# Kernel optimization log

Hardware: AMD Instinct MI355X
Metric: run time of the kernel (lower is better)

## Reference

```python
import jax, jax.numpy as jnp
import numpy as np

B, C, D_EMB = 512, 100000, 128
SCALE = 3.0
EPS = 1e-5


def _l2norm(x, eps=1e-12):
    # matches torch F.normalize(p=2, dim=-1)
    n = jnp.sqrt(jnp.sum(x * x, axis=-1, keepdims=True))
    return x / jnp.maximum(n, eps)


def setup_inputs() -> dict:
    key = jax.random.key(0)
    k1, k2, k3 = jax.random.split(key, 3)
    X = jax.random.normal(k1, (B, D_EMB), dtype=jnp.float32)
    indices = jnp.arange(B, dtype=jnp.int64)
    T = jax.random.randint(k2, (B,), 0, C).astype(jnp.int64)
    proxies = jax.random.normal(k3, (C, D_EMB), dtype=jnp.float32) / 8.0
    return {"X": X, "indices": indices, "T": T, "proxies": proxies}


def reference(X, indices, T, proxies):
    P = _l2norm(proxies)            # (C, D)
    Xn = _l2norm(X)                 # (B, D)

    # cross_attention -----------------------------------------------------
    Pb = P[T]                       # (B, D) gather of class proxies
    # affinity2boundary[b,k] = relu(<(Pb[b]+Pb[k])/2, Xn[k]>)
    #   = relu(0.5 * ((Pb @ Xn.T)[b,k] + diag[k]))  -- avoids (B,B,D) intermediate
    diag = jnp.sum(Pb * Xn, axis=-1)                       # (B,)
    aff2b = jax.nn.relu(0.5 * (Pb @ Xn.T + diag[None, :]))  # (B, B)
    aff2x = jax.nn.relu(Xn @ Xn.T)                          # (B, B)
    attention = aff2b + aff2x

    # NOTE: faithful to torch broadcasting: (B,B) / (B,) divides by COLUMN sums
    attention = attention / (attention.sum(-1) + EPS)       # (B, B)
    attention_weights = attention @ Xn                      # (B, D)
    X2 = Xn + attention_weights

    Ps = SCALE * _l2norm(P)         # (C, D), rows have norm SCALE
    Xs = SCALE * _l2norm(X2)        # (B, D)

    # squared pairwise distance block between X rows and proxy rows
    sx = jnp.sum(Xs * Xs, axis=-1)  # (B,)
    sp = jnp.sum(Ps * Ps, axis=-1)  # (C,)
    Dm = jnp.maximum(sx[:, None] + sp[None, :] - 2.0 * (Xs @ Ps.T), 0.0)  # (B, C)

    # one-hot targets (smoothing_const = 0) with masked log-softmax
    lsm = jax.nn.log_softmax(-Dm, axis=-1)                  # (B, C)
    loss = -lsm[jnp.arange(B), T]                           # (B,)
    return loss.mean()
```

## Files before the change

### kernel.cpp

```cpp
#include <hip/hip_runtime.h>
#include <hip/hip_bf16.h>
#include <math.h>

#define B_N 512
#define C_N 100000
#define CPAD 100032
#define D_N 128
#define NCHUNK (CPAD / 64)
#define K6_GX 256
#define K6_BLOCKS K6_GX
#define PAD_CORR (32.0f * 1.522998e-8f)

typedef short short8 __attribute__((ext_vector_type(8)));
typedef float f32x4 __attribute__((ext_vector_type(4)));

__device__ __forceinline__ unsigned short f2bf(float f) {
  unsigned int u = __float_as_uint(f);
  u += 0x7fffu + ((u >> 16) & 1u);
  return (unsigned short)(u >> 16);
}

__device__ __forceinline__ unsigned int pk2bf(float lo, float hi) {
  return (unsigned int)f2bf(lo) | ((unsigned int)f2bf(hi) << 16);
}

__device__ __forceinline__ void gl_lds16(const void* g, void* l) {
  __builtin_amdgcn_global_load_lds(
      (const __attribute__((address_space(1))) void*)g,
      (__attribute__((address_space(3))) void*)l, 16, 0, 0);
}

template <int NT>
__device__ __forceinline__ float block_reduce_sum(float v, float* red) {
  int t = threadIdx.x;
  __syncthreads();
  red[t] = v;
  __syncthreads();
#pragma unroll
  for (int s = NT / 2; s > 0; s >>= 1) {
    if (t < s) red[t] += red[t + s];
    __syncthreads();
  }
  return red[0];
}

__global__ __launch_bounds__(256) void kX(const float* __restrict__ X,
                                          const float* __restrict__ proxies,
                                          const int* __restrict__ T,
                                          float* __restrict__ Xn, float* __restrict__ Pb,
                                          float* __restrict__ diagv,
                                          int* __restrict__ ctrs) {
  __shared__ float red[256];
  int b = blockIdx.x;
  int t = threadIdx.x;
  bool act = t < D_N;
  float v = act ? X[b * D_N + t] : 0.f;
  float ss = block_reduce_sum<256>(v * v, red);
  float xn = v / fmaxf(sqrtf(ss), 1e-12f);
  if (act) Xn[b * D_N + t] = xn;
  int row = T[b];
  float p = act ? proxies[(size_t)row * D_N + t] : 0.f;
  float ss2 = block_reduce_sum<256>(p * p, red);
  float pn = p / fmaxf(sqrtf(ss2), 1e-12f);
  if (act) Pb[b * D_N + t] = pn;
  float d = block_reduce_sum<256>(pn * xn, red);
  if (t == 0) {
    diagv[b] = d;
    if (b == 0) ctrs[32] = 0;
  }
}

__global__ __launch_bounds__(512) void k3_att(const float* __restrict__ Xn,
                                              const float* __restrict__ Pb,
                                              const float* __restrict__ diagv,
                                              float* __restrict__ A, float* __restrict__ S) {
  __shared__ float xb[128], pbv[128];
  __shared__ float red[512];
  int b = blockIdx.x, t = threadIdx.x;
  if (t < 128) {
    xb[t] = Xn[b * D_N + t];
    pbv[t] = Pb[b * D_N + t];
  }
  __syncthreads();
  const float4* xr = (const float4*)(Xn + (size_t)t * D_N);
  float d1 = 0.f, d2 = 0.f;
#pragma unroll
  for (int i = 0; i < 32; i++) {
    float4 v = xr[i];
    d1 += pbv[4 * i] * v.x + pbv[4 * i + 1] * v.y + pbv[4 * i + 2] * v.z + pbv[4 * i + 3] * v.w;
    d2 += xb[4 * i] * v.x + xb[4 * i + 1] * v.y + xb[4 * i + 2] * v.z + xb[4 * i + 3] * v.w;
  }
  float a = fmaxf(0.5f * (d1 + diagv[t]), 0.f) + fmaxf(d2, 0.f);
  A[(size_t)b * B_N + t] = a;
  float rs = block_reduce_sum<512>(a, red);
  if (t == 0) S[b] = rs;
}

__global__ __launch_bounds__(512) void k4ab(const float* __restrict__ Xn,
                                            const float* __restrict__ Pb,
                                            const float* __restrict__ A,
                                            const float* __restrict__ S,
                                            unsigned short* __restrict__ Xsb,
                                            float* __restrict__ lossT,
                                            float* __restrict__ sumexpP) {
  __shared__ float xb[128], pbv[128];
  __shared__ float aw[512];
  __shared__ float red[512];
  int b = blockIdx.x, t = threadIdx.x;
  if (t < 128) {
    xb[t] = Xn[b * D_N + t];
    pbv[t] = Pb[b * D_N + t];
  }
  aw[t] = A[(size_t)b * B_N + t] / (S[t] + 1e-5f);
  __syncthreads();

  int d = t & 127, h = t >> 7;
  const float* xp = Xn + (size_t)(128 * h) * D_N + d;
  const float* awp = aw + 128 * h;
  float a0 = 0.f, a1 = 0.f, a2 = 0.f, a3 = 0.f;
#pragma unroll 8
  for (int kk = 0; kk < 128; kk += 4) {
    a0 = fmaf(awp[kk], xp[(size_t)kk * D_N], a0);
    a1 = fmaf(awp[kk + 1], xp[(size_t)(kk + 1) * D_N], a1);
    a2 = fmaf(awp[kk + 2], xp[(size_t)(kk + 2) * D_N], a2);
    a3 = fmaf(awp[kk + 3], xp[(size_t)(kk + 3) * D_N], a3);
  }
  red[t] = (a0 + a1) + (a2 + a3);
  __syncthreads();
  float x2 = (t < 128) ? (xb[t] + red[t] + red[t + 128] + red[t + 256] + red[t + 384]) : 0.f;

  float ss = block_reduce_sum<512>(x2 * x2, red);
  float xs = 3.f * x2 / fmaxf(sqrtf(ss), 1e-12f);
  if (t < 128) Xsb[b * D_N + t] = f2bf(xs);
  float dt = block_reduce_sum<512>((t < 128) ? xs * pbv[t] : 0.f, red);
  if (t == 0) {
    lossT[b] = fmaxf(18.f - 6.f * dt, 0.f);
    sumexpP[b * 16] = 0.f;
  }
}

__global__ __launch_bounds__(512, 2) void k6_big(const float* __restrict__ proxies,
                                                 const unsigned short* __restrict__ Xsb,
                                                 float* __restrict__ sumexpP,
                                                 const float* __restrict__ lossT,
                                                 int* __restrict__ ctrs,
                                                 float* __restrict__ out) {
  __shared__ __align__(16) float fP[2][64 * 128];
  __shared__ __align__(16) unsigned short sP[64 * 128];
  __shared__ float redf[512];
  __shared__ int sLast;
  const int t = threadIdx.x;
  const int w = t >> 6;
  const int lane = t & 63;
  const int lc = lane & 15;
  const int q = lane >> 4;

  short8 afr[4][4];
#pragma unroll
  for (int mt = 0; mt < 4; mt++)
#pragma unroll
    for (int ks = 0; ks < 4; ks++)
      afr[mt][ks] = *(const short8*)(Xsb + (size_t)(64 * w + 16 * mt + lc) * D_N +
                                     ks * 32 + q * 8);

  float pe[4][4];
#pragma unroll
  for (int mt = 0; mt < 4; mt++)
#pragma unroll
    for (int r = 0; r < 4; r++) pe[mt][r] = 0.f;

  const int srow = 8 * w + (lane >> 5);
  const int scol = (lane & 31) * 4;
#define STAGEF(c0_, buf_)                                                             \
  {                                                                                   \
    _Pragma("unroll") for (int j = 0; j < 4; j++) {                                   \
      int gr = (c0_) + srow + 2 * j;                                                  \
      gr = gr < C_N ? gr : (C_N - 1);               \
      gl_lds16(proxies + (size_t)gr * D_N + scol,                                     \
               &fP[buf_][(8 * w + 2 * j) * D_N]);                                     \
    }                                                                                 \
  }

  const int cr = t >> 3;
  const int cs = t & 7;

  int cc = blockIdx.x;
  STAGEF(cc * 64, 0);
  int buf = 0;
  while (true) {
    int nc = cc + gridDim.x;
    if (nc < NCHUNK) {
      STAGEF(nc * 64, buf ^ 1);
      __builtin_amdgcn_sched_barrier(0);
      __builtin_amdgcn_s_waitcnt(0x0F74);
    } else {
      __builtin_amdgcn_sched_barrier(0);
      __builtin_amdgcn_s_waitcnt(0x0F70);
    }
    __builtin_amdgcn_sched_barrier(0);

    {
      const float* src = &fP[buf][cr * D_N + cs * 16];
      float4 v0 = ((const float4*)src)[0];
      float4 v1 = ((const float4*)src)[1];
      float4 v2 = ((const float4*)src)[2];
      float4 v3 = ((const float4*)src)[3];
      float s0 = v0.x * v0.x + v0.y * v0.y + v0.z * v0.z + v0.w * v0.w;
      float s1 = v1.x * v1.x + v1.y * v1.y + v1.z * v1.z + v1.w * v1.w;
      float s2 = v2.x * v2.x + v2.y * v2.y + v2.z * v2.z + v2.w * v2.w;
      float s3 = v3.x * v3.x + v3.y * v3.y + v3.z * v3.z + v3.w * v3.w;
      float ss = (s0 + s1) + (s2 + s3);
      ss += __shfl_xor(ss, 1);
      ss += __shfl_xor(ss, 2);
      ss += __shfl_xor(ss, 4);
      float inv = 1.f / fmaxf(sqrtf(ss), 1e-12f);
      if (cc * 64 + cr >= C_N) inv = 0.f;
      uint4 g0, g1;
      g0.x = pk2bf(v0.x * inv, v0.y * inv);
      g0.y = pk2bf(v0.z * inv, v0.w * inv);
      g0.z = pk2bf(v1.x * inv, v1.y * inv);
      g0.w = pk2bf(v1.z * inv, v1.w * inv);
      g1.x = pk2bf(v2.x * inv, v2.y * inv);
      g1.y = pk2bf(v2.z * inv, v2.w * inv);
      g1.z = pk2bf(v3.x * inv, v3.y * inv);
      g1.w = pk2bf(v3.z * inv, v3.w * inv);
      int P0 = (2 * cs) ^ (cr & 15);
      int P1 = (2 * cs + 1) ^ (cr & 15);
      *(uint4*)&sP[cr * D_N + P0 * 8] = g0;
      *(uint4*)&sP[cr * D_N + P1 * 8] = g1;
    }
    __builtin_amdgcn_s_waitcnt(0xC07F);
    __builtin_amdgcn_s_barrier();
    __builtin_amdgcn_sched_barrier(0);

    f32x4 acc[4][4];
#pragma unroll
    for (int mt = 0; mt < 4; mt++)
#pragma unroll
      for (int nt = 0; nt < 4; nt++) acc[mt][nt] = (f32x4){0.f, 0.f, 0.f, 0.f};

#pragma unroll
    for (int ks = 0; ks < 4; ks++) {
      short8 bfr[4];
#pragma unroll
      for (int nt = 0; nt < 4; nt++) {
        int R = 16 * nt + lc;
        int g = (ks * 4 + q) ^ lc;
        bfr[nt] = *(const short8*)(&sP[R * 128 + (g << 3)]);
      }
#pragma unroll
      for (int nt = 0; nt < 4; nt++)
#pragma unroll
        for (int mt = 0; mt < 4; mt++)
          acc[mt][nt] = __builtin_amdgcn_mfma_f32_16x16x32_bf16(afr[mt][ks], bfr[nt],
                                                                acc[mt][nt], 0, 0, 0);
    }

#pragma unroll
    for (int mt = 0; mt < 4; mt++)
#pragma unroll
      for (int nt = 0; nt < 4; nt++) {
        f32x4 a = acc[mt][nt];
#pragma unroll
        for (int r = 0; r < 4; r++)
          pe[mt][r] += __builtin_amdgcn_exp2f(
              fminf(__fmaf_rn(8.65617024533378f, a[r], -25.9685107360013f), 0.f));
      }

    if (nc >= NCHUNK) break;
    __builtin_amdgcn_sched_barrier(0);
    __builtin_amdgcn_s_barrier();
    cc = nc;
    buf ^= 1;
  }

#pragma unroll
  for (int mt = 0; mt < 4; mt++) {
#pragma unroll
    for (int r = 0; r < 4; r++) {
      float p = pe[mt][r];
      p += __shfl_xor(p, 1);
      p += __shfl_xor(p, 2);
      p += __shfl_xor(p, 4);
      p += __shfl_xor(p, 8);
      if (lc == 0) {
        int rb = 64 * w + 16 * mt + 4 * q + r;
        atomicAdd(&sumexpP[rb * 16], p);
      }
    }
  }

  __builtin_amdgcn_s_waitcnt(0);
  if (t == 0) sLast = atomicAdd(&ctrs[32], 1);
  __syncthreads();
  if (sLast == K6_BLOCKS - 1) {
    float se = __hip_atomic_load(&sumexpP[t * 16], __ATOMIC_RELAXED,
                                 __HIP_MEMORY_SCOPE_AGENT);
    float v = lossT[t] + logf(se - PAD_CORR);
    float s = block_reduce_sum<512>(v, redf);
    if (t == 0) out[0] = s * (1.0f / 512.0f);
  }
}

extern "C" void kernel_launch(void* const* d_in, const int* in_sizes, int n_in,
                              void* d_out, int out_size, void* d_ws, size_t ws_size,
                              hipStream_t stream) {
  const float* X = (const float*)d_in[0];
  const int* T = (const int*)d_in[2];
  const float* proxies = (const float*)d_in[3];
  float* out = (float*)d_out;

  char* ws = (char*)d_ws;
  float* Xn = (float*)(ws + (size_t)CPAD * D_N * 2);
  float* Pb = Xn + B_N * D_N;
  float* X2 = Pb + B_N * D_N;
  float* dg = X2 + B_N * D_N;
  float* S = dg + B_N;
  float* lossT = S + B_N;
  float* sumexpP = lossT + B_N;
  unsigned short* Xsb = (unsigned short*)(sumexpP + B_N * 16);
  float* A = (float*)(Xsb + B_N * D_N);
  int* ctrs = (int*)(A + B_N * B_N);

  kX<<<B_N, 256, 0, stream>>>(X, proxies, T, Xn, Pb, dg, ctrs);
  k3_att<<<B_N, 512, 0, stream>>>(Xn, Pb, dg, A, S);
  k4ab<<<B_N, 512, 0, stream>>>(Xn, Pb, A, S, Xsb, lossT, sumexpP);
  k6_big<<<K6_GX, 512, 0, stream>>>(proxies, Xsb, sumexpP, lossT, ctrs, out);
}
```

Measured before the change: 142.3 us.

## Double-buffer bf16 proxy tile, assign contiguous chunks, shrink accumulators and kX block

The bf16 proxy tile in LDS now has two buffers, so the trailing barrier at the end of each chunk iteration can be dropped. Each block now handles a fixed, contiguous range of 6 or 7 chunks instead of a grid-strided sequence. The MFMA loop now runs with the column tile outermost, so only 4 accumulators are live at a time and the exp-sum epilogue is applied per column tile, which lowers register pressure. kX now launches 128 threads instead of 256, removing idle lanes. The extra LDS buffer costs 16 KB per block, which could limit how many blocks fit on a CU.

```diff
diff --git a/kernel.cpp b/kernel.cpp
--- a/kernel.cpp
+++ b/kernel.cpp
@@ -44,26 +44,25 @@
   return red[0];
 }
 
-__global__ __launch_bounds__(256) void kX(const float* __restrict__ X,
+__global__ __launch_bounds__(128) void kX(const float* __restrict__ X,
                                           const float* __restrict__ proxies,
                                           const int* __restrict__ T,
                                           float* __restrict__ Xn, float* __restrict__ Pb,
                                           float* __restrict__ diagv,
                                           int* __restrict__ ctrs) {
-  __shared__ float red[256];
+  __shared__ float red[128];
   int b = blockIdx.x;
   int t = threadIdx.x;
-  bool act = t < D_N;
-  float v = act ? X[b * D_N + t] : 0.f;
-  float ss = block_reduce_sum<256>(v * v, red);
+  float v = X[b * D_N + t];
+  float ss = block_reduce_sum<128>(v * v, red);
   float xn = v / fmaxf(sqrtf(ss), 1e-12f);
-  if (act) Xn[b * D_N + t] = xn;
+  Xn[b * D_N + t] = xn;
   int row = T[b];
-  float p = act ? proxies[(size_t)row * D_N + t] : 0.f;
-  float ss2 = block_reduce_sum<256>(p * p, red);
+  float p = proxies[(size_t)row * D_N + t];
+  float ss2 = block_reduce_sum<128>(p * p, red);
   float pn = p / fmaxf(sqrtf(ss2), 1e-12f);
-  if (act) Pb[b * D_N + t] = pn;
-  float d = block_reduce_sum<256>(pn * xn, red);
+  Pb[b * D_N + t] = pn;
+  float d = block_reduce_sum<128>(pn * xn, red);
   if (t == 0) {
     diagv[b] = d;
     if (b == 0) ctrs[32] = 0;
@@ -146,7 +145,7 @@
                                                  int* __restrict__ ctrs,
                                                  float* __restrict__ out) {
   __shared__ __align__(16) float fP[2][64 * 128];
-  __shared__ __align__(16) unsigned short sP[64 * 128];
+  __shared__ __align__(16) unsigned short sP[2][64 * 128];
   __shared__ float redf[512];
   __shared__ int sLast;
   const int t = threadIdx.x;
@@ -184,13 +183,16 @@
   const int cr = t >> 3;
   const int cs = t & 7;
 
-  int cc = blockIdx.x;
-  STAGEF(cc * 64, 0);
-  int buf = 0;
-  while (true) {
-    int nc = cc + gridDim.x;
-    if (nc < NCHUNK) {
-      STAGEF(nc * 64, buf ^ 1);
+  const int bid = blockIdx.x;
+  const int start = bid * 6 + (bid < 27 ? bid : 27);
+  const int nch = 6 + (bid < 27 ? 1 : 0);
+
+  STAGEF(start * 64, 0);
+  int fbuf = 0, sbuf = 0;
+  for (int k = 0; k < nch; k++) {
+    const int cc = start + k;
+    if (k + 1 < nch) {
+      STAGEF((cc + 1) * 64, fbuf ^ 1);
       __builtin_amdgcn_sched_barrier(0);
       __builtin_amdgcn_s_waitcnt(0x0F74);
     } else {
@@ -200,7 +202,7 @@
     __builtin_amdgcn_sched_barrier(0);
 
     {
-      const float* src = &fP[buf][cr * D_N + cs * 16];
+      const float* src = &fP[fbuf][cr * D_N + cs * 16];
       float4 v0 = ((const float4*)src)[0];
       float4 v1 = ((const float4*)src)[1];
       float4 v2 = ((const float4*)src)[2];
@@ -226,52 +228,40 @@
       g1.w = pk2bf(v3.z * inv, v3.w * inv);
       int P0 = (2 * cs) ^ (cr & 15);
       int P1 = (2 * cs + 1) ^ (cr & 15);
-      *(uint4*)&sP[cr * D_N + P0 * 8] = g0;
-      *(uint4*)&sP[cr * D_N + P1 * 8] = g1;
+      *(uint4*)&sP[sbuf][cr * D_N + P0 * 8] = g0;
+      *(uint4*)&sP[sbuf][cr * D_N + P1 * 8] = g1;
     }
     __builtin_amdgcn_s_waitcnt(0xC07F);
     __builtin_amdgcn_s_barrier();
     __builtin_amdgcn_sched_barrier(0);
 
-    f32x4 acc[4][4];
-#pragma unroll
-    for (int mt = 0; mt < 4; mt++)
-#pragma unroll
-      for (int nt = 0; nt < 4; nt++) acc[mt][nt] = (f32x4){0.f, 0.f, 0.f, 0.f};
-
-#pragma unroll
-    for (int ks = 0; ks < 4; ks++) {
+#pragma unroll
+    for (int nt = 0; nt < 4; nt++) {
       short8 bfr[4];
 #pragma unroll
-      for (int nt = 0; nt < 4; nt++) {
+      for (int ks = 0; ks < 4; ks++) {
         int R = 16 * nt + lc;
         int g = (ks * 4 + q) ^ lc;
-        bfr[nt] = *(const short8*)(&sP[R * 128 + (g << 3)]);
+        bfr[ks] = *(const short8*)(&sP[sbuf][R * 128 + (g << 3)]);
       }
-#pragma unroll
-      for (int nt = 0; nt < 4; nt++)
+      f32x4 acc[4];
+#pragma unroll
+      for (int mt = 0; mt < 4; mt++) acc[mt] = (f32x4){0.f, 0.f, 0.f, 0.f};
+#pragma unroll
+      for (int ks = 0; ks < 4; ks++)
 #pragma unroll
         for (int mt = 0; mt < 4; mt++)
-          acc[mt][nt] = __builtin_amdgcn_mfma_f32_16x16x32_bf16(afr[mt][ks], bfr[nt],
-                                                                acc[mt][nt], 0, 0, 0);
-    }
-
-#pragma unroll
-    for (int mt = 0; mt < 4; mt++)
-#pragma unroll
-      for (int nt = 0; nt < 4; nt++) {
-        f32x4 a = acc[mt][nt];
+          acc[mt] = __builtin_amdgcn_mfma_f32_16x16x32_bf16(afr[mt][ks], bfr[ks],
+                                                            acc[mt], 0, 0, 0);
+#pragma unroll
+      for (int mt = 0; mt < 4; mt++)
 #pragma unroll
         for (int r = 0; r < 4; r++)
           pe[mt][r] += __builtin_amdgcn_exp2f(
-              fminf(__fmaf_rn(8.65617024533378f, a[r], -25.9685107360013f), 0.f));
-      }
-
-    if (nc >= NCHUNK) break;
-    __builtin_amdgcn_sched_barrier(0);
-    __builtin_amdgcn_s_barrier();
-    cc = nc;
-    buf ^= 1;
+              fminf(__fmaf_rn(8.65617024533378f, acc[mt][r], -25.9685107360013f), 0.f));
+    }
+    fbuf ^= 1;
+    sbuf ^= 1;
   }
 
 #pragma unroll
@@ -322,7 +312,7 @@
   float* A = (float*)(Xsb + B_N * D_N);
   int* ctrs = (int*)(A + B_N * B_N);
 
-  kX<<<B_N, 256, 0, stream>>>(X, proxies, T, Xn, Pb, dg, ctrs);
+  kX<<<B_N, 128, 0, stream>>>(X, proxies, T, Xn, Pb, dg, ctrs);
   k3_att<<<B_N, 512, 0, stream>>>(Xn, Pb, dg, A, S);
   k4ab<<<B_N, 512, 0, stream>>>(Xn, Pb, A, S, Xsb, lossT, sumexpP);
   k6_big<<<K6_GX, 512, 0, stream>>>(proxies, Xsb, sumexpP, lossT, ctrs, out);
```

After: 141.8 us. Within noise of the previous version (-0.3%).
